# Performance work log

Measured on AMD Instinct MI355X. Metric: run time of the kernel, lower is better.

The kernel has to match this reference:

```python
import jax, jax.numpy as jnp
import numpy as np

B, S, D, H, KV, HD = 2, 2048, 1024, 16, 4, 64
NUM_BUCKETS, MAX_DIST = 32, 128


def _rel_pos_bucket(rel_pos, num_buckets=NUM_BUCKETS, max_distance=MAX_DIST):
    # bidirectional (is_decoder=False) T5 bucketing
    nb = num_buckets // 2
    buckets = (rel_pos > 0).astype(jnp.int32) * nb
    rel = jnp.abs(rel_pos)
    max_exact = nb // 2
    is_small = rel < max_exact
    rel_f = jnp.maximum(rel, 1).astype(jnp.float32)
    large = max_exact + (
        jnp.log(rel_f / max_exact) / np.log(max_distance / max_exact) * (nb - max_exact)
    ).astype(jnp.int32)
    large = jnp.minimum(large, nb - 1)
    return buckets + jnp.where(is_small, rel, large)


def _pool_weight(W, scale, apply_scale):
    # W: [inner_dim, d_model] (torch Linear layout). Optionally scale per head,
    # group-sum heads into kv_heads, broadcast back to n_heads.
    Wh = W.reshape(H, HD, D)                       # [H, hd, D]
    if apply_scale:
        # torch path: W.T -> [D,H,hd] * scale[H,1] -> back; equivalent per-head scale
        Wh = Wh * scale[:, :, None]                # scale: [H,1] -> [H,1,1]
    Wg = Wh.reshape(KV, H // KV, HD, D).sum(axis=1)  # [KV, hd, D]
    Wb = jnp.repeat(Wg, H // KV, axis=0)           # [H, hd, D]
    return Wb.reshape(H * HD, D)


def setup_inputs() -> dict:
    key = jax.random.key(0)
    ks = jax.random.split(key, 8)
    s = 1.0 / np.sqrt(D)
    return {
        "hidden_states": jax.random.normal(ks[0], (B, S, D), jnp.float32),
        "Wq": jax.random.normal(ks[1], (H * HD, D), jnp.float32) * s,
        "Wk": jax.random.normal(ks[2], (H * HD, D), jnp.float32) * s,
        "Wv": jax.random.normal(ks[3], (H * HD, D), jnp.float32) * s,
        "Wo": jax.random.normal(ks[4], (D, H * HD), jnp.float32) * s,
        "key_scale": jax.random.normal(ks[5], (H, 1), jnp.float32),
        "value_scale": jax.random.normal(ks[6], (H, 1), jnp.float32),
        "bias_emb": jax.random.normal(ks[7], (NUM_BUCKETS, H), jnp.float32),
    }


def reference(hidden_states, Wq, Wk, Wv, Wo, key_scale, value_scale, bias_emb):
    x = hidden_states
    # Q projection -> [B, H, S, hd]
    q = (x @ Wq.T).reshape(B, S, H, HD).transpose(0, 2, 1, 3)

    # K weight: per-head scale applied, then pooled. V weight: the original code
    # computes the scaled version but then (bug, replicated faithfully) pools the
    # RAW v weight, so value_scale has no effect on the forward math.
    Wk_eff = _pool_weight(Wk, key_scale, apply_scale=True)
    Wv_eff = _pool_weight(Wv, value_scale, apply_scale=False)

    k = (x @ Wk_eff.T).reshape(B, S, H, HD).transpose(0, 2, 1, 3)
    v = (x @ Wv_eff.T).reshape(B, S, H, HD).transpose(0, 2, 1, 3)

    # T5 attention: no 1/sqrt(d) scaling
    scores = jnp.einsum("bhqd,bhkd->bhqk", q, k)  # [B,H,S,S]

    # relative position bias
    ctx = jnp.arange(S)[:, None]
    mem = jnp.arange(S)[None, :]
    buckets = _rel_pos_bucket(mem - ctx)            # [S, S]
    pos_bias = bias_emb[buckets]                    # [S, S, H]
    pos_bias = pos_bias.transpose(2, 0, 1)[None]    # [1, H, S, S]

    scores = scores + pos_bias
    attn = jax.nn.softmax(scores.astype(jnp.float32), axis=-1).astype(scores.dtype)
    out = jnp.einsum("bhqk,bhkd->bhqd", attn, v)    # [B,H,S,hd]
    out = out.transpose(0, 2, 1, 3).reshape(B, S, H * HD)
    return out @ Wo.T                               # [B, S, D]
```

## Files before the change

kernel.cpp:

```cpp
#include <hip/hip_runtime.h>

using half8 = __attribute__((ext_vector_type(8))) _Float16;
using half4 = __attribute__((ext_vector_type(4))) _Float16;
using f32x4 = __attribute__((ext_vector_type(4))) float;

#define BB 2
#define SS 2048
#define DD 1024
#define HH 16
#define KVH 4
#define HDIM 64
#define NQK 1280

#define GLDS(g, l) __builtin_amdgcn_global_load_lds( \
    (const __attribute__((address_space(1))) void*)(g), \
    (__attribute__((address_space(3))) void*)(l), 16, 0, 0)

__device__ __forceinline__ f32x4 mfma16(half4 a, half4 b, f32x4 c) {
    return __builtin_amdgcn_mfma_f32_16x16x16f16(a, b, c, 0, 0, 0);
}

__global__ void prep_weights(const float* __restrict__ Wq, const float* __restrict__ Wk,
                             const float* __restrict__ Wv, const float* __restrict__ Wo,
                             const float* __restrict__ ksc,
                             _Float16* __restrict__ Wqk, _Float16* __restrict__ Wvb,
                             _Float16* __restrict__ Wob)
{
    int row = blockIdx.x;
    int c = threadIdx.x * 4;
    if (row < NQK) {
        if (row < 1024) {
            #pragma unroll
            for (int j = 0; j < 4; ++j)
                Wqk[(size_t)row * DD + c + j] = (_Float16)Wq[(size_t)row * DD + c + j];
        } else {
            int kh = row - 1024;
            int kvi = kh >> 6, hd = kh & 63;
            #pragma unroll
            for (int j = 0; j < 4; ++j) {
                float s = 0.f;
                #pragma unroll
                for (int g = 0; g < 4; ++g)
                    s += Wk[(size_t)((kvi * 4 + g) * 64 + hd) * DD + c + j] * ksc[kvi * 4 + g];
                Wqk[(size_t)row * DD + c + j] = (_Float16)s;
            }
        }
    } else if (row < 1536) {
        int vh = row - 1280;
        int kvi = vh >> 6, hd = vh & 63;
        #pragma unroll
        for (int j = 0; j < 4; ++j) {
            float s = 0.f;
            #pragma unroll
            for (int g = 0; g < 4; ++g)
                s += Wv[(size_t)((kvi * 4 + g) * 64 + hd) * DD + c + j];
            Wvb[(size_t)vh * DD + c + j] = (_Float16)s;
        }
    } else {
        int r = row - 1536;
        #pragma unroll
        for (int j = 0; j < 4; ++j)
            Wob[(size_t)r * DD + c + j] = (_Float16)Wo[(size_t)r * DD + c + j];
    }
}

__global__ void cast_x(const float* __restrict__ X, _Float16* __restrict__ Xh)
{
    int idx = (blockIdx.x * 256 + threadIdx.x) * 4;
    float4 v = *(const float4*)(X + idx);
    half4 o = { (_Float16)v.x, (_Float16)v.y, (_Float16)v.z, (_Float16)v.w };
    *(half4*)(Xh + idx) = o;
}

__device__ __forceinline__ int rel_large(int rel) {
    int n;
    if (rel < 12) n = 0; else if (rel < 16) n = 1; else if (rel < 23) n = 2;
    else if (rel < 32) n = 3; else if (rel < 46) n = 4; else if (rel < 64) n = 5;
    else if (rel < 91) n = 6; else if (rel < 128) n = 7; else n = 8;
    int large = 8 + n;
    return large > 15 ? 15 : large;
}

__global__ void build_bias(const float* __restrict__ bias_emb, float* __restrict__ tab)
{
    int idx = blockIdx.x * 256 + threadIdx.x;
    if (idx >= HH * 4095) return;
    int h = idx / 4095;
    int dpos = idx % 4095;
    int d = dpos - 2047;
    int rel = d < 0 ? -d : d;
    int bucket = (rel < 8) ? rel : rel_large(rel);
    if (d > 0) bucket += 16;
    tab[(size_t)h * 4095 + dpos] = bias_emb[bucket * HH + h];
}

template<int OUTK>
__global__ __launch_bounds__(256) void gemm_bt(const _Float16* __restrict__ A,
                                               const _Float16* __restrict__ B,
                                               void* __restrict__ C0,
                                               _Float16* __restrict__ C1,
                                               int M, int K, int ldc)
{
    __shared__ __align__(16) _Float16 As[128 * 32];
    __shared__ __align__(16) _Float16 Bs[128 * 32];
    int m0 = blockIdx.y * 128, n0 = blockIdx.x * 128;
    int t = threadIdx.x;
    int wv = t >> 6, lane = t & 63;
    int wm = wv >> 1, wn = wv & 1;
    int lr = lane & 15, lg = lane >> 4;
    int srow = lane >> 2;
    int scol = (lane & 3) << 3;
    f32x4 acc[4][4] = {};

    for (int k0 = 0; k0 < K; k0 += 32) {
        __syncthreads();
        #pragma unroll
        for (int i = 0; i < 2; ++i) {
            int chunk = wv * 2 + i;
            int row = chunk * 16 + srow;
            GLDS(A + (size_t)(m0 + row) * K + k0 + scol, As + chunk * 512 + lane * 8);
            GLDS(B + (size_t)(n0 + row) * K + k0 + scol, Bs + chunk * 512 + lane * 8);
        }
        __syncthreads();
        half8 af[4], bfr[4];
        #pragma unroll
        for (int mi = 0; mi < 4; ++mi)
            af[mi] = *(const half8*)(&As[(wm * 64 + mi * 16 + lr) * 32 + lg * 8]);
        #pragma unroll
        for (int ni = 0; ni < 4; ++ni)
            bfr[ni] = *(const half8*)(&Bs[(wn * 64 + ni * 16 + lr) * 32 + lg * 8]);
        __builtin_amdgcn_s_setprio(1);
        #pragma unroll
        for (int mi = 0; mi < 4; ++mi)
            #pragma unroll
            for (int ni = 0; ni < 4; ++ni)
                acc[mi][ni] = __builtin_amdgcn_mfma_f32_16x16x32_f16(af[mi], bfr[ni], acc[mi][ni], 0, 0, 0);
        __builtin_amdgcn_s_setprio(0);
    }

    #pragma unroll
    for (int mi = 0; mi < 4; ++mi) {
        #pragma unroll
        for (int ni = 0; ni < 4; ++ni) {
            int rowb = m0 + wm * 64 + mi * 16 + 4 * lg;
            int col  = n0 + wn * 64 + ni * 16 + lr;
            if constexpr (OUTK == 0) {
                #pragma unroll
                for (int r = 0; r < 4; ++r)
                    ((float*)C0)[(size_t)(rowb + r) * ldc + col] = acc[mi][ni][r];
            } else {
                if (n0 < 1280) {
                    #pragma unroll
                    for (int r = 0; r < 4; ++r)
                        ((_Float16*)C0)[(size_t)(rowb + r) * ldc + col] = (_Float16)acc[mi][ni][r];
                } else {
                    half4 o = { (_Float16)acc[mi][ni][0], (_Float16)acc[mi][ni][1],
                                (_Float16)acc[mi][ni][2], (_Float16)acc[mi][ni][3] };
                    *(half4*)(C1 + (size_t)(col - 1280) * M + rowb) = o;
                }
            }
        }
    }
}

__global__ __launch_bounds__(256) void attn(const _Float16* __restrict__ Y,
                                            const _Float16* __restrict__ Vt,
                                            const float* __restrict__ tab,
                                            _Float16* __restrict__ O)
{
    int blk = (blockIdx.x & 7) * 128 + (blockIdx.x >> 3);
    int qb = blk & 31, h = (blk >> 5) & 15, b = blk >> 9;
    int kv = h >> 2;
    int q0 = qb * 64;
    int t = threadIdx.x, w = t >> 6, lane = t & 63, lr = lane & 15, lg = lane >> 4;

    __shared__ __align__(16) _Float16 Ks[2][64 * 72];
    __shared__ __align__(16) _Float16 Vst[2][64 * 72];
    __shared__ float bias_s[2][128];

    const size_t yoff = (size_t)(b * SS + q0 + w * 16 + lr) * NQK + h * 64;
    half8 aq0 = *(const half8*)(Y + yoff + lg * 8);
    half8 aq1 = *(const half8*)(Y + yoff + 32 + lg * 8);

    const float bias_neg = tab[(size_t)h * 4095 + 0];
    const float bias_pos = tab[(size_t)h * 4095 + 4094];

    f32x4 acc_o[4] = {};
    float m = -1e30f, l = 0.f;
    const int bb = 63 - w * 16 - lr + 4 * lg;

    uint4 kreg0, kreg1, vreg0, vreg1;
    float breg = 0.f;
    const int srow = t >> 3, sc8 = (t & 7) << 3;
    const int srow1 = srow + 32;

#define ATTN_LOAD(KEY0)                                                          \
    {                                                                            \
        int k0_ = (KEY0);                                                        \
        kreg0 = *(const uint4*)(Y + (size_t)(b * SS + k0_ + srow)  * NQK + 1024 + kv * 64 + sc8); \
        kreg1 = *(const uint4*)(Y + (size_t)(b * SS + k0_ + srow1) * NQK + 1024 + kv * 64 + sc8); \
        vreg0 = *(const uint4*)(Vt + (size_t)(kv * 64 + srow)  * 4096 + b * SS + k0_ + sc8); \
        vreg1 = *(const uint4*)(Vt + (size_t)(kv * 64 + srow1) * 4096 + b * SS + k0_ + sc8); \
        bool far_ = (k0_ >= q0 + 192) || (k0_ <= q0 - 192);                      \
        if (!far_ && t < 128) {                                                  \
            int ti = k0_ - q0 + t - 63 + 2047;                                   \
            ti = ti < 0 ? 0 : (ti > 4094 ? 4094 : ti);                           \
            breg = tab[(size_t)h * 4095 + ti];                                   \
        }                                                                        \
    }

#define ATTN_WRITE(BUF, KEY0)                                                    \
    {                                                                            \
        int bf_ = (BUF);                                                         \
        *(uint4*)(&Ks[bf_][srow  * 72 + sc8]) = kreg0;                           \
        *(uint4*)(&Ks[bf_][srow1 * 72 + sc8]) = kreg1;                           \
        *(uint4*)(&Vst[bf_][srow  * 72 + sc8]) = vreg0;                          \
        *(uint4*)(&Vst[bf_][srow1 * 72 + sc8]) = vreg1;                          \
        bool far_ = ((KEY0) >= q0 + 192) || ((KEY0) <= q0 - 192);                \
        if (!far_ && t < 128) bias_s[bf_][t] = breg;                             \
    }

    ATTN_LOAD(0);
    ATTN_WRITE(0, 0);
    __syncthreads();
    int cur = 0;

    for (int key0 = 0; key0 < SS; key0 += 64) {
        if (key0 + 64 < SS) ATTN_LOAD(key0 + 64);

        const _Float16* ks = Ks[cur];
        const _Float16* vs = Vst[cur];
        bool far = (key0 >= q0 + 192) || (key0 <= q0 - 192);

        f32x4 z = {0.f, 0.f, 0.f, 0.f};
        f32x4 sc[4];
        __builtin_amdgcn_s_setprio(1);
        #pragma unroll
        for (int dt = 0; dt < 4; ++dt) {
            half8 bk0 = *(const half8*)(&ks[(dt * 16 + lr) * 72 + lg * 8]);
            half8 bk1 = *(const half8*)(&ks[(dt * 16 + lr) * 72 + 32 + lg * 8]);
            sc[dt] = __builtin_amdgcn_mfma_f32_16x16x32_f16(bk0, aq0, z, 0, 0, 0);
            sc[dt] = __builtin_amdgcn_mfma_f32_16x16x32_f16(bk1, aq1, sc[dt], 0, 0, 0);
        }
        __builtin_amdgcn_s_setprio(0);

        float c;
        if (!far) {
            #pragma unroll
            for (int dt = 0; dt < 4; ++dt)
                #pragma unroll
                for (int r = 0; r < 4; ++r)
                    sc[dt][r] += bias_s[cur][bb + dt * 16 + r];
            c = 0.f;
        } else {
            c = (key0 > q0) ? bias_pos : bias_neg;
        }

        float pmax = sc[0][0];
        #pragma unroll
        for (int dt = 0; dt < 4; ++dt)
            #pragma unroll
            for (int r = 0; r < 4; ++r) pmax = fmaxf(pmax, sc[dt][r]);
        pmax = fmaxf(pmax, __shfl_xor(pmax, 16, 64));
        pmax = fmaxf(pmax, __shfl_xor(pmax, 32, 64));
        pmax += c;
        if (__any(pmax > m + 8.f)) {
            float mn = fmaxf(m, pmax);
            float scale = __expf(m - mn);
            l *= scale;
            #pragma unroll
            for (int odt = 0; odt < 4; ++odt)
                #pragma unroll
                for (int r = 0; r < 4; ++r) acc_o[odt][r] *= scale;
            m = mn;
        }
        float moff = m - c;
        float rs = 0.f;
        #pragma unroll
        for (int dt = 0; dt < 4; ++dt)
            #pragma unroll
            for (int r = 0; r < 4; ++r) {
                float p = __expf(sc[dt][r] - moff);
                sc[dt][r] = p;
                rs += p;
            }
        rs += __shfl_xor(rs, 16, 64);
        rs += __shfl_xor(rs, 32, 64);
        l += rs;

        half4 pf[4];
        #pragma unroll
        for (int dt = 0; dt < 4; ++dt)
            pf[dt] = { (_Float16)sc[dt][0], (_Float16)sc[dt][1],
                       (_Float16)sc[dt][2], (_Float16)sc[dt][3] };

        __builtin_amdgcn_s_setprio(1);
        #pragma unroll
        for (int odt = 0; odt < 4; ++odt)
            #pragma unroll
            for (int dt = 0; dt < 4; ++dt) {
                half4 vf = *(const half4*)(&vs[(odt * 16 + lr) * 72 + dt * 16 + 4 * lg]);
                acc_o[odt] = mfma16(vf, pf[dt], acc_o[odt]);
            }
        __builtin_amdgcn_s_setprio(0);

        if (key0 + 64 < SS) {
            ATTN_WRITE(cur ^ 1, key0 + 64);
            __syncthreads();
            cur ^= 1;
        }
    }

    float inv = 1.f / l;
    _Float16* orow = O + (size_t)(b * SS + q0 + w * 16 + lr) * 1024 + h * 64;
    #pragma unroll
    for (int odt = 0; odt < 4; ++odt) {
        half4 o = { (_Float16)(acc_o[odt][0] * inv), (_Float16)(acc_o[odt][1] * inv),
                    (_Float16)(acc_o[odt][2] * inv), (_Float16)(acc_o[odt][3] * inv) };
        *(half4*)(orow + odt * 16 + 4 * lg) = o;
    }
#undef ATTN_LOAD
#undef ATTN_WRITE
}

extern "C" void kernel_launch(void* const* d_in, const int* in_sizes, int n_in,
                              void* d_out, int out_size, void* d_ws, size_t ws_size,
                              hipStream_t stream)
{
    const float* x   = (const float*)d_in[0];
    const float* Wq  = (const float*)d_in[1];
    const float* Wk  = (const float*)d_in[2];
    const float* Wv  = (const float*)d_in[3];
    const float* Wo  = (const float*)d_in[4];
    const float* ksc = (const float*)d_in[5];
    const float* bias_emb = (const float*)d_in[7];
    float* out = (float*)d_out;

    char* ws = (char*)d_ws;
    _Float16* Wqk = (_Float16*)(ws);
    _Float16* Wvb = (_Float16*)(ws + 2621440);
    _Float16* Wob = (_Float16*)(ws + 3145728);
    float*    tab = (float*)(ws + 5242880);
    _Float16* Xh  = (_Float16*)(ws + 5505024);
    _Float16* Y   = (_Float16*)(ws + 13893632);
    _Float16* Vt  = (_Float16*)(ws + 24379392);
    _Float16* Ob  = (_Float16*)(ws + 26476544);

    prep_weights<<<2560, 256, 0, stream>>>(Wq, Wk, Wv, Wo, ksc, Wqk, Wvb, Wob);
    cast_x<<<4096, 256, 0, stream>>>(x, Xh);
    build_bias<<<256, 256, 0, stream>>>(bias_emb, tab);

    gemm_bt<3><<<dim3(12, 32), 256, 0, stream>>>(Xh, Wqk, Y, Vt, 4096, 1024, NQK);

    attn<<<1024, 256, 0, stream>>>(Y, Vt, tab, Ob);

    gemm_bt<0><<<dim3(8, 32), 256, 0, stream>>>(Ob, Wob, out, nullptr, 4096, 1024, 1024);
}
```

Measured before the change: 145.0 us.

## Fuse prep kernels, double-buffer GEMM LDS, swizzle blocks, use exp2 softmax

Merges the three preprocessing kernels into one launch to cut launch overhead. The GEMM gets double-buffered LDS tiles so the next k-slice's global-to-LDS load overlaps the current MFMAs, plus a block-index swizzle to improve L2 locality. Attention softmax switches to exp2 by folding log2(e) into Wq and the bias table, and uses packed f16 conversion for the probabilities. Risks include doubled LDS use lowering occupancy and slight precision changes from the pre-scaled fp16 Q weights.

After: 133.5 us. 1.09x faster.

```diff
diff --git a/kernel.cpp b/kernel.cpp
--- a/kernel.cpp
+++ b/kernel.cpp
@@ -1,8 +1,10 @@
 #include <hip/hip_runtime.h>
 
-using half8 = __attribute__((ext_vector_type(8))) _Float16;
-using half4 = __attribute__((ext_vector_type(4))) _Float16;
-using f32x4 = __attribute__((ext_vector_type(4))) float;
+using half8  = __attribute__((ext_vector_type(8))) _Float16;
+using half4  = __attribute__((ext_vector_type(4))) _Float16;
+using half2v = __attribute__((ext_vector_type(2))) _Float16;
+using fp16x2 = __attribute__((ext_vector_type(2))) __fp16;
+using f32x4  = __attribute__((ext_vector_type(4))) float;
 
 #define BB 2
 #define SS 2048
@@ -11,6 +13,7 @@
 #define KVH 4
 #define HDIM 64
 #define NQK 1280
+#define LOG2E 1.4426950408889634f
 
 #define GLDS(g, l) __builtin_amdgcn_global_load_lds( \
     (const __attribute__((address_space(1))) void*)(g), \
@@ -20,56 +23,17 @@
     return __builtin_amdgcn_mfma_f32_16x16x16f16(a, b, c, 0, 0, 0);
 }
 
-__global__ void prep_weights(const float* __restrict__ Wq, const float* __restrict__ Wk,
-                             const float* __restrict__ Wv, const float* __restrict__ Wo,
-                             const float* __restrict__ ksc,
-                             _Float16* __restrict__ Wqk, _Float16* __restrict__ Wvb,
-                             _Float16* __restrict__ Wob)
-{
-    int row = blockIdx.x;
-    int c = threadIdx.x * 4;
-    if (row < NQK) {
-        if (row < 1024) {
-            #pragma unroll
-            for (int j = 0; j < 4; ++j)
-                Wqk[(size_t)row * DD + c + j] = (_Float16)Wq[(size_t)row * DD + c + j];
-        } else {
-            int kh = row - 1024;
-            int kvi = kh >> 6, hd = kh & 63;
-            #pragma unroll
-            for (int j = 0; j < 4; ++j) {
-                float s = 0.f;
-                #pragma unroll
-                for (int g = 0; g < 4; ++g)
-                    s += Wk[(size_t)((kvi * 4 + g) * 64 + hd) * DD + c + j] * ksc[kvi * 4 + g];
-                Wqk[(size_t)row * DD + c + j] = (_Float16)s;
-            }
-        }
-    } else if (row < 1536) {
-        int vh = row - 1280;
-        int kvi = vh >> 6, hd = vh & 63;
-        #pragma unroll
-        for (int j = 0; j < 4; ++j) {
-            float s = 0.f;
-            #pragma unroll
-            for (int g = 0; g < 4; ++g)
-                s += Wv[(size_t)((kvi * 4 + g) * 64 + hd) * DD + c + j];
-            Wvb[(size_t)vh * DD + c + j] = (_Float16)s;
-        }
-    } else {
-        int r = row - 1536;
-        #pragma unroll
-        for (int j = 0; j < 4; ++j)
-            Wob[(size_t)r * DD + c + j] = (_Float16)Wo[(size_t)r * DD + c + j];
-    }
-}
-
-__global__ void cast_x(const float* __restrict__ X, _Float16* __restrict__ Xh)
-{
-    int idx = (blockIdx.x * 256 + threadIdx.x) * 4;
-    float4 v = *(const float4*)(X + idx);
-    half4 o = { (_Float16)v.x, (_Float16)v.y, (_Float16)v.z, (_Float16)v.w };
-    *(half4*)(Xh + idx) = o;
+__device__ __forceinline__ float fexp2(float x) {
+#if __has_builtin(__builtin_amdgcn_exp2f)
+    return __builtin_amdgcn_exp2f(x);
+#else
+    return exp2f(x);
+#endif
+}
+
+__device__ __forceinline__ half2v cvt_pk_f16(float a, float b) {
+    fp16x2 r = __builtin_amdgcn_cvt_pkrtz(a, b);
+    return __builtin_bit_cast(half2v, r);
 }
 
 __device__ __forceinline__ int rel_large(int rel) {
@@ -81,17 +45,69 @@
     return large > 15 ? 15 : large;
 }
 
-__global__ void build_bias(const float* __restrict__ bias_emb, float* __restrict__ tab)
+__global__ void prep_all(const float* __restrict__ x,
+                         const float* __restrict__ Wq, const float* __restrict__ Wk,
+                         const float* __restrict__ Wv, const float* __restrict__ Wo,
+                         const float* __restrict__ ksc, const float* __restrict__ bias_emb,
+                         _Float16* __restrict__ Wqk, _Float16* __restrict__ Wvb,
+                         _Float16* __restrict__ Wob, float* __restrict__ tab,
+                         _Float16* __restrict__ Xh)
 {
-    int idx = blockIdx.x * 256 + threadIdx.x;
-    if (idx >= HH * 4095) return;
-    int h = idx / 4095;
-    int dpos = idx % 4095;
-    int d = dpos - 2047;
-    int rel = d < 0 ? -d : d;
-    int bucket = (rel < 8) ? rel : rel_large(rel);
-    if (d > 0) bucket += 16;
-    tab[(size_t)h * 4095 + dpos] = bias_emb[bucket * HH + h];
+    int bid = blockIdx.x;
+    if (bid < 2560) {
+        int row = bid;
+        int c = threadIdx.x * 4;
+        if (row < NQK) {
+            if (row < 1024) {
+                #pragma unroll
+                for (int j = 0; j < 4; ++j)
+                    Wqk[(size_t)row * DD + c + j] = (_Float16)(Wq[(size_t)row * DD + c + j] * LOG2E);
+            } else {
+                int kh = row - 1024;
+                int kvi = kh >> 6, hd = kh & 63;
+                #pragma unroll
+                for (int j = 0; j < 4; ++j) {
+                    float s = 0.f;
+                    #pragma unroll
+                    for (int g = 0; g < 4; ++g)
+                        s += Wk[(size_t)((kvi * 4 + g) * 64 + hd) * DD + c + j] * ksc[kvi * 4 + g];
+                    Wqk[(size_t)row * DD + c + j] = (_Float16)s;
+                }
+            }
+        } else if (row < 1536) {
+            int vh = row - 1280;
+            int kvi = vh >> 6, hd = vh & 63;
+            #pragma unroll
+            for (int j = 0; j < 4; ++j) {
+                float s = 0.f;
+                #pragma unroll
+                for (int g = 0; g < 4; ++g)
+                    s += Wv[(size_t)((kvi * 4 + g) * 64 + hd) * DD + c + j];
+                Wvb[(size_t)vh * DD + c + j] = (_Float16)s;
+            }
+        } else {
+            int r = row - 1536;
+            #pragma unroll
+            for (int j = 0; j < 4; ++j)
+                Wob[(size_t)r * DD + c + j] = (_Float16)Wo[(size_t)r * DD + c + j];
+        }
+    } else if (bid < 6656) {
+        int idx = ((bid - 2560) * 256 + threadIdx.x) * 4;
+        float4 v = *(const float4*)(x + idx);
+        half4 o = { (_Float16)v.x, (_Float16)v.y, (_Float16)v.z, (_Float16)v.w };
+        *(half4*)(Xh + idx) = o;
+    } else {
+        int idx = (bid - 6656) * 256 + threadIdx.x;
+        if (idx < HH * 4095) {
+            int h = idx / 4095;
+            int dpos = idx % 4095;
+            int d = dpos - 2047;
+            int rel = d < 0 ? -d : d;
+            int bucket = (rel < 8) ? rel : rel_large(rel);
+            if (d > 0) bucket += 16;
+            tab[(size_t)h * 4095 + dpos] = bias_emb[bucket * HH + h] * LOG2E;
+        }
+    }
 }
 
 template<int OUTK>
@@ -101,9 +117,14 @@
                                                _Float16* __restrict__ C1,
                                                int M, int K, int ldc)
 {
-    __shared__ __align__(16) _Float16 As[128 * 32];
-    __shared__ __align__(16) _Float16 Bs[128 * 32];
-    int m0 = blockIdx.y * 128, n0 = blockIdx.x * 128;
+    __shared__ __align__(16) _Float16 As[2][128 * 32];
+    __shared__ __align__(16) _Float16 Bs[2][128 * 32];
+
+    int nwg = gridDim.x * gridDim.y;
+    int lid = blockIdx.y * gridDim.x + blockIdx.x;
+    int sid = (lid & 7) * (nwg >> 3) + (lid >> 3);
+    int m0 = (sid / gridDim.x) * 128, n0 = (sid % gridDim.x) * 128;
+
     int t = threadIdx.x;
     int wv = t >> 6, lane = t & 63;
     int wm = wv >> 1, wn = wv & 1;
@@ -112,23 +133,32 @@
     int scol = (lane & 3) << 3;
     f32x4 acc[4][4] = {};
 
+#define GSTAGE(BUF, K0)                                                       \
+    {                                                                         \
+        _Pragma("unroll")                                                     \
+        for (int i_ = 0; i_ < 2; ++i_) {                                      \
+            int chunk_ = wv * 2 + i_;                                         \
+            int row_ = chunk_ * 16 + srow;                                    \
+            GLDS(A + (size_t)(m0 + row_) * K + (K0) + scol,                   \
+                 &As[BUF][chunk_ * 512 + lane * 8]);                          \
+            GLDS(B + (size_t)(n0 + row_) * K + (K0) + scol,                   \
+                 &Bs[BUF][chunk_ * 512 + lane * 8]);                          \
+        }                                                                     \
+    }
+
+    GSTAGE(0, 0);
+    __syncthreads();
+    int cur = 0;
+
     for (int k0 = 0; k0 < K; k0 += 32) {
-        __syncthreads();
-        #pragma unroll
-        for (int i = 0; i < 2; ++i) {
-            int chunk = wv * 2 + i;
-            int row = chunk * 16 + srow;
-            GLDS(A + (size_t)(m0 + row) * K + k0 + scol, As + chunk * 512 + lane * 8);
-            GLDS(B + (size_t)(n0 + row) * K + k0 + scol, Bs + chunk * 512 + lane * 8);
-        }
-        __syncthreads();
+        if (k0 + 32 < K) GSTAGE(cur ^ 1, k0 + 32);
         half8 af[4], bfr[4];
         #pragma unroll
         for (int mi = 0; mi < 4; ++mi)
-            af[mi] = *(const half8*)(&As[(wm * 64 + mi * 16 + lr) * 32 + lg * 8]);
+            af[mi] = *(const half8*)(&As[cur][(wm * 64 + mi * 16 + lr) * 32 + lg * 8]);
         #pragma unroll
         for (int ni = 0; ni < 4; ++ni)
-            bfr[ni] = *(const half8*)(&Bs[(wn * 64 + ni * 16 + lr) * 32 + lg * 8]);
+            bfr[ni] = *(const half8*)(&Bs[cur][(wn * 64 + ni * 16 + lr) * 32 + lg * 8]);
         __builtin_amdgcn_s_setprio(1);
         #pragma unroll
         for (int mi = 0; mi < 4; ++mi)
@@ -136,7 +166,10 @@
             for (int ni = 0; ni < 4; ++ni)
                 acc[mi][ni] = __builtin_amdgcn_mfma_f32_16x16x32_f16(af[mi], bfr[ni], acc[mi][ni], 0, 0, 0);
         __builtin_amdgcn_s_setprio(0);
-    }
+        __syncthreads();
+        cur ^= 1;
+    }
+#undef GSTAGE
 
     #pragma unroll
     for (int mi = 0; mi < 4; ++mi) {
@@ -266,7 +299,7 @@
         pmax += c;
         if (__any(pmax > m + 8.f)) {
             float mn = fmaxf(m, pmax);
-            float scale = __expf(m - mn);
+            float scale = fexp2(m - mn);
             l *= scale;
             #pragma unroll
             for (int odt = 0; odt < 4; ++odt)
@@ -280,7 +313,7 @@
         for (int dt = 0; dt < 4; ++dt)
             #pragma unroll
             for (int r = 0; r < 4; ++r) {
-                float p = __expf(sc[dt][r] - moff);
+                float p = fexp2(sc[dt][r] - moff);
                 sc[dt][r] = p;
                 rs += p;
             }
@@ -290,9 +323,11 @@
 
         half4 pf[4];
         #pragma unroll
-        for (int dt = 0; dt < 4; ++dt)
-            pf[dt] = { (_Float16)sc[dt][0], (_Float16)sc[dt][1],
-                       (_Float16)sc[dt][2], (_Float16)sc[dt][3] };
+        for (int dt = 0; dt < 4; ++dt) {
+            half2v p01 = cvt_pk_f16(sc[dt][0], sc[dt][1]);
+            half2v p23 = cvt_pk_f16(sc[dt][2], sc[dt][3]);
+            pf[dt] = { p01[0], p01[1], p23[0], p23[1] };
+        }
 
         __builtin_amdgcn_s_setprio(1);
         #pragma unroll
@@ -346,9 +381,8 @@
     _Float16* Vt  = (_Float16*)(ws + 24379392);
     _Float16* Ob  = (_Float16*)(ws + 26476544);
 
-    prep_weights<<<2560, 256, 0, stream>>>(Wq, Wk, Wv, Wo, ksc, Wqk, Wvb, Wob);
-    cast_x<<<4096, 256, 0, stream>>>(x, Xh);
-    build_bias<<<256, 256, 0, stream>>>(bias_emb, tab);
+    prep_all<<<6912, 256, 0, stream>>>(x, Wq, Wk, Wv, Wo, ksc, bias_emb,
+                                       Wqk, Wvb, Wob, tab, Xh);
 
     gemm_bt<3><<<dim3(12, 32), 256, 0, stream>>>(Xh, Wqk, Y, Vt, 4096, 1024, NQK);
 
```
